# Optimization experiments

Hardware: AMD Instinct MI355X
Metric: run time of the kernel (lower is better)

Reference implementation:

```python
import jax, jax.numpy as jnp
import numpy as np

NHID = 1024
NTOKEN = 10000
T, B = 128, 32
INITRANGE = 0.04
# DARTS recurrent genotype: (activation, predecessor-state index)
GENO = (("sigmoid", 0), ("relu", 1), ("relu", 1), ("identity", 1),
        ("tanh", 2), ("sigmoid", 5), ("tanh", 3), ("relu", 5))
CONCAT = tuple(range(1, 9))
ACT = {"sigmoid": jax.nn.sigmoid, "relu": jax.nn.relu,
       "tanh": jnp.tanh, "identity": lambda x: x}


def setup_inputs() -> dict:
    key = jax.random.key(0)
    ks = jax.random.split(key, 4)
    u = lambda k, shape: jax.random.uniform(k, shape, jnp.float32, -INITRANGE, INITRANGE)
    return {
        "tokens": jax.random.randint(ks[0], (T, B), 0, NTOKEN),
        "h0": jnp.zeros((B, NHID), jnp.float32),
        "enc_W": u(ks[1], (NTOKEN, NHID)),            # tied encoder/decoder weight
        "W0": u(ks[2], (2 * NHID, 2 * NHID)),          # (ninp+nhid, 2*nhid)
        "Ws": u(ks[3], (len(GENO), NHID, 2 * NHID)),   # one matrix per genotype edge
        "dec_b": jnp.zeros((NTOKEN,), jnp.float32),
    }


def _cell(x, h_prev, W0, Ws):
    # init state: c0,h0 from cat(x, h_prev) @ W0
    xh = jnp.concatenate([x, h_prev], axis=-1)           # (B, 2*nhid)
    c0, h0 = jnp.split(xh @ W0, 2, axis=-1)
    s = h_prev + jax.nn.sigmoid(c0) * (jnp.tanh(h0) - h_prev)
    states = [s]
    for i, (name, pred) in enumerate(GENO):
        sp = states[pred]
        c, h = jnp.split(sp @ Ws[i], 2, axis=-1)
        states.append(sp + jax.nn.sigmoid(c) * (ACT[name](h) - sp))
    # output = mean over concat states
    return sum(states[i] for i in CONCAT) / float(len(CONCAT))


def reference(tokens, h0, enc_W, W0, Ws, dec_b):
    emb = enc_W[tokens]                                  # (T, B, ninp)

    def step(h, x):
        h_new = _cell(x, h, W0, Ws)
        return h_new, h_new

    h_last, hiddens = jax.lax.scan(step, h0, emb)        # hiddens: (T, B, nhid)
    logits = hiddens @ enc_W.T + dec_b                   # tied decoder (T, B, ntoken)
    log_prob = jax.nn.log_softmax(logits, axis=-1)
    return log_prob, h_last[None]                        # ((T,B,V), (1,B,nhid))
```

## Files before the change

### kernel.cpp

```cpp
#include <hip/hip_runtime.h>
#include <cmath>

#define NHID 1024
#define NTOK 10000
#define TT 128
#define BB 32
#define BN (BB*NHID)
#define WMAT (2048*1024)
#define FSTRIDE 16

typedef __attribute__((ext_vector_type(8))) short s8v;
typedef __attribute__((ext_vector_type(4))) float f4v;

#define MFMA(a,b,c) __builtin_amdgcn_mfma_f32_16x16x32_bf16(a,b,c,0,0,0)

__device__ __forceinline__ float sigf(float x){ return 1.f/(1.f+__expf(-x)); }
__device__ __forceinline__ float actf(int a, float h){
  switch(a){ case 0: return sigf(h); case 1: return fmaxf(h,0.f);
             case 2: return tanhf(h); default: return h; }
}
__device__ __forceinline__ unsigned short f2bf(float x){
  union { float f; unsigned u; } v; v.f = x;
  unsigned r = v.u + 0x7fffu + ((v.u >> 16) & 1u);
  return (unsigned short)(r >> 16);
}

__device__ __forceinline__ void ld_f2(const float* p, float& x0, float& x1){
  unsigned long long u = __hip_atomic_load((const unsigned long long*)p,
                         __ATOMIC_RELAXED, __HIP_MEMORY_SCOPE_AGENT);
  union { unsigned long long u; float f[2]; } v; v.u = u;
  x0 = v.f[0]; x1 = v.f[1];
}

__device__ __forceinline__ void coh_ld16(const unsigned short* pa, const unsigned short* pb,
                                         s8v A[8], s8v B[8]){
  asm volatile(
    "global_load_dwordx4 %0, %16, off sc0 sc1\n\t"
    "global_load_dwordx4 %1, %16, off offset:64 sc0 sc1\n\t"
    "global_load_dwordx4 %2, %16, off offset:128 sc0 sc1\n\t"
    "global_load_dwordx4 %3, %16, off offset:192 sc0 sc1\n\t"
    "global_load_dwordx4 %4, %16, off offset:256 sc0 sc1\n\t"
    "global_load_dwordx4 %5, %16, off offset:320 sc0 sc1\n\t"
    "global_load_dwordx4 %6, %16, off offset:384 sc0 sc1\n\t"
    "global_load_dwordx4 %7, %16, off offset:448 sc0 sc1\n\t"
    "global_load_dwordx4 %8, %17, off sc0 sc1\n\t"
    "global_load_dwordx4 %9, %17, off offset:64 sc0 sc1\n\t"
    "global_load_dwordx4 %10, %17, off offset:128 sc0 sc1\n\t"
    "global_load_dwordx4 %11, %17, off offset:192 sc0 sc1\n\t"
    "global_load_dwordx4 %12, %17, off offset:256 sc0 sc1\n\t"
    "global_load_dwordx4 %13, %17, off offset:320 sc0 sc1\n\t"
    "global_load_dwordx4 %14, %17, off offset:384 sc0 sc1\n\t"
    "global_load_dwordx4 %15, %17, off offset:448 sc0 sc1\n\t"
    "s_waitcnt vmcnt(0)"
    : "=&v"(A[0]),"=&v"(A[1]),"=&v"(A[2]),"=&v"(A[3]),
      "=&v"(A[4]),"=&v"(A[5]),"=&v"(A[6]),"=&v"(A[7]),
      "=&v"(B[0]),"=&v"(B[1]),"=&v"(B[2]),"=&v"(B[3]),
      "=&v"(B[4]),"=&v"(B[5]),"=&v"(B[6]),"=&v"(B[7])
    : "v"(pa), "v"(pb)
    : "memory");
}

__device__ __forceinline__ void st_wt32(void* p, unsigned x){
  asm volatile("global_store_dword %0, %1, off sc0 sc1" :: "v"(p), "v"(x) : "memory");
}
__device__ __forceinline__ void st_wt64(void* p, unsigned long long x){
  asm volatile("global_store_dwordx2 %0, %1, off sc0 sc1" :: "v"(p), "v"(x) : "memory");
}
__device__ __forceinline__ unsigned long long packf2(float a, float b){
  union { float f[2]; unsigned long long u; } v; v.f[0]=a; v.f[1]=b; return v.u;
}


__global__ __launch_bounds__(256) void k_transpose_cvt(
    const float* __restrict__ W0, const float* __restrict__ Ws,
    unsigned short* __restrict__ dstAll)
{
  int z = blockIdx.z;
  const float* src = (z==0) ? W0 : (z==1) ? (W0 + (size_t)1024*2048)
                                          : (Ws + (size_t)(z-2)*1024*2048);
  unsigned short* dst = dstAll + (size_t)z*WMAT;
  __shared__ float tile[32][33];
  int n0 = blockIdx.x*32;
  int k0 = blockIdx.y*32;
  int tx = threadIdx.x & 31, ty = threadIdx.x >> 5;
  #pragma unroll
  for (int i=0;i<4;i++){
    int k = k0 + ty + i*8;
    tile[ty + i*8][tx] = src[(size_t)k*2048 + n0 + tx];
  }
  __syncthreads();
  #pragma unroll
  for (int i=0;i<4;i++){
    int n = n0 + ty + i*8;
    dst[(size_t)n*1024 + k0 + tx] = f2bf(tile[tx][ty + i*8]);
  }
}

__global__ void k_cvt(const float* __restrict__ src, unsigned short* __restrict__ dst, int n){
  int i = blockIdx.x*blockDim.x + threadIdx.x;
  int stride = gridDim.x*blockDim.x;
  for (; i < n; i += stride) dst[i] = f2bf(src[i]);
}

__global__ void k_zero(unsigned* __restrict__ p, int n){
  int i = blockIdx.x*blockDim.x + threadIdx.x;
  if (i < n) p[i] = 0u;
}


__device__ __forceinline__ void poll1(const unsigned* F, int idx, unsigned tgt){
  const unsigned* f = F + (size_t)idx*FSTRIDE;
  while (__hip_atomic_load(f, __ATOMIC_RELAXED, __HIP_MEMORY_SCOPE_AGENT) < tgt)
    __builtin_amdgcn_s_sleep(2);
}
__device__ __forceinline__ void signal(unsigned* F, int s, int tile, unsigned val){
  asm volatile("s_waitcnt vmcnt(0)" ::: "memory");
  __syncthreads();
  if (threadIdx.x == 0)
    st_wt32((void*)(F + (size_t)((s<<6)+tile)*FSTRIDE), val);
}

struct B8 { s8v c[8]; s8v h[8]; };

__device__ __forceinline__ void load_b8(const unsigned short* __restrict__ Wt,
                                        int z, int j0, int r, int kb, int q, B8& B){
  const unsigned short* wz = Wt + (size_t)z*WMAT;
  const s8v* bc = (const s8v*)(wz + (size_t)(j0+r)*1024 + kb);
  const s8v* bh = (const s8v*)(wz + (size_t)(1024+j0+r)*1024 + kb);
  #pragma unroll
  for (int i=0;i<8;i++){ B.c[i]=bc[q+4*i]; B.h[i]=bh[q+4*i]; }
}

__device__ __forceinline__ void do_edge_reg(
    const B8& B, float* __restrict__ st_f,
    unsigned short* __restrict__ st_bf, float* __restrict__ red,
    unsigned* __restrict__ F, int pred, int outs, int act,
    int j0, int tile, unsigned tgt, int wave, int q, int r, int tid)
{
  int lane = tid & 63;
  if (lane < 17){
    int idx = (pred<<6) + ((lane<16) ? (wave*16 + lane) : tile);
    poll1(F, idx, tgt);
  }
  int row = tid>>3, col = (tid&7)*2;
  size_t off = (size_t)row*NHID + j0 + col;
  float sp0, sp1;
  ld_f2(st_f + (size_t)pred*BN + off, sp0, sp1);
  const unsigned short* spb = st_bf + (size_t)pred*BN;
  int kb = wave*256;
  s8v a0[8], a1[8];
  coh_ld16(spb + (size_t)r*NHID + kb + q*8,
           spb + (size_t)(16+r)*NHID + kb + q*8, a0, a1);
  f4v zz = {0.f,0.f,0.f,0.f};
  f4v aC0=zz,aC1=zz,aH0=zz,aH1=zz;
  #pragma unroll
  for (int i=0;i<8;i++){
    aC0=MFMA(a0[i],B.c[i],aC0); aC1=MFMA(a1[i],B.c[i],aC1);
    aH0=MFMA(a0[i],B.h[i],aH0); aH1=MFMA(a1[i],B.h[i],aH1);
  }
  #pragma unroll
  for (int i=0;i<4;i++){
    red[((wave*4+0)*32 + q*4+i)*16 + r]    = aC0[i];
    red[((wave*4+0)*32 + 16+q*4+i)*16 + r] = aC1[i];
    red[((wave*4+1)*32 + q*4+i)*16 + r]    = aH0[i];
    red[((wave*4+1)*32 + 16+q*4+i)*16 + r] = aH1[i];
  }
  __syncthreads();
  float cs0=0,cs1=0,hs0=0,hs1=0;
  #pragma unroll
  for (int w2=0; w2<4; w2++){
    cs0 += red[((w2*4+0)*32+row)*16+col];
    cs1 += red[((w2*4+0)*32+row)*16+col+1];
    hs0 += red[((w2*4+1)*32+row)*16+col];
    hs1 += red[((w2*4+1)*32+row)*16+col+1];
  }
  float v0 = sp0 + sigf(cs0)*(actf(act,hs0) - sp0);
  float v1 = sp1 + sigf(cs1)*(actf(act,hs1) - sp1);
  st_wt64(&st_f[(size_t)outs*BN+off], packf2(v0, v1));
  unsigned pk = (unsigned)f2bf(v0) | ((unsigned)f2bf(v1)<<16);
  st_wt32((unsigned*)(st_bf + (size_t)outs*BN + off), pk);
  signal(F, outs, tile, tgt);
}

__global__ __launch_bounds__(256, 1) void k_recur(
    const int* __restrict__ tok, const float* __restrict__ h0f,
    const unsigned short* __restrict__ encb,
    const unsigned short* __restrict__ Wt,
    const unsigned short* __restrict__ h0b,
    float* __restrict__ st_f, unsigned short* __restrict__ st_bf,
    float* __restrict__ h_f, unsigned short* __restrict__ h_bf,
    unsigned short* __restrict__ hid_bf, unsigned* __restrict__ F)
{
  __shared__ float red[4*4*32*16];
  int wg = blockIdx.x, grp = wg >> 6, tile = wg & 63;
  int tid = threadIdx.x, wave = tid>>6, lane = tid&63, q = lane>>4, r = lane&15;
  int j0 = tile * 16;

  if (grp == 0) {
    B8 BX; load_b8(Wt, 0, j0, r, wave*256, q, BX);
    B8 BH; load_b8(Wt, 1, j0, r, wave*256, q, BH);
    B8 B3; load_b8(Wt, 5, j0, r, wave*256, q, B3);

    for (int t = 0; t < TT; ++t) {
      unsigned tgt = t+1;
      s8v xa0[8], xa1[8];
      {
        int kb = wave * 256;
        const s8v* e0p = (const s8v*)(encb + (size_t)tok[t*BB + r]*NHID + kb);
        const s8v* e1p = (const s8v*)(encb + (size_t)tok[t*BB + 16 + r]*NHID + kb);
        #pragma unroll
        for (int i=0;i<8;i++){ xa0[i]=e0p[q+4*i]; xa1[i]=e1p[q+4*i]; }
      }
      if (t && lane < 17){
        int idx = (8<<6) + ((lane<16) ? (wave*16 + lane) : tile);
        poll1(F, idx, t);
      }
      int row = tid>>3, col = (tid&7)*2;
      size_t off = (size_t)row*NHID + j0 + col;
      const float* hfb = t ? h_f : h0f;
      float hp0, hp1; ld_f2(hfb + off, hp0, hp1);
      const unsigned short* hb = t ? h_bf : h0b;
      int kb = wave*256;
      s8v ha0[8], ha1[8];
      coh_ld16(hb + (size_t)r*NHID + kb + q*8,
               hb + (size_t)(16+r)*NHID + kb + q*8, ha0, ha1);
      f4v zz = {0.f,0.f,0.f,0.f};
      f4v aC0=zz,aC1=zz,aH0=zz,aH1=zz;
      #pragma unroll
      for (int i=0;i<8;i++){
        aC0=MFMA(xa0[i],BX.c[i],aC0); aC1=MFMA(xa1[i],BX.c[i],aC1);
        aH0=MFMA(xa0[i],BX.h[i],aH0); aH1=MFMA(xa1[i],BX.h[i],aH1);
      }
      #pragma unroll
      for (int i=0;i<8;i++){
        aC0=MFMA(ha0[i],BH.c[i],aC0); aC1=MFMA(ha1[i],BH.c[i],aC1);
        aH0=MFMA(ha0[i],BH.h[i],aH0); aH1=MFMA(ha1[i],BH.h[i],aH1);
      }
      #pragma unroll
      for (int i=0;i<4;i++){
        red[((wave*4+0)*32 + q*4+i)*16 + r]    = aC0[i];
        red[((wave*4+0)*32 + 16+q*4+i)*16 + r] = aC1[i];
        red[((wave*4+1)*32 + q*4+i)*16 + r]    = aH0[i];
        red[((wave*4+1)*32 + 16+q*4+i)*16 + r] = aH1[i];
      }
      __syncthreads();
      float cs0=0,cs1=0,hs0=0,hs1=0;
      #pragma unroll
      for (int w2=0; w2<4; w2++){
        cs0 += red[((w2*4+0)*32+row)*16+col];
        cs1 += red[((w2*4+0)*32+row)*16+col+1];
        hs0 += red[((w2*4+1)*32+row)*16+col];
        hs1 += red[((w2*4+1)*32+row)*16+col+1];
      }
      float v0 = hp0 + sigf(cs0)*(tanhf(hs0)-hp0);
      float v1 = hp1 + sigf(cs1)*(tanhf(hs1)-hp1);
      st_wt64(&st_f[off], packf2(v0, v1));
      unsigned pk = (unsigned)f2bf(v0) | ((unsigned)f2bf(v1)<<16);
      st_wt32((unsigned*)(st_bf + off), pk);
      signal(F, 0, tile, tgt);
      do_edge_reg(B3, st_f, st_bf, red, F, 1, 4, 3, j0, tile, tgt, wave, q, r, tid);
    }
  } else if (grp == 1) {
    B8 B0; load_b8(Wt, 2, j0, r, wave*256, q, B0);
    B8 B4; load_b8(Wt, 6, j0, r, wave*256, q, B4);
    for (int t = 0; t < TT; ++t) {
      unsigned tgt = t+1;
      do_edge_reg(B0, st_f, st_bf, red, F, 0, 1, 0, j0, tile, tgt, wave, q, r, tid);
      do_edge_reg(B4, st_f, st_bf, red, F, 2, 5, 2, j0, tile, tgt, wave, q, r, tid);
    }
  } else if (grp == 2) {
    B8 B1; load_b8(Wt, 3, j0, r, wave*256, q, B1);
    B8 B6; load_b8(Wt, 8, j0, r, wave*256, q, B6);
    for (int t = 0; t < TT; ++t) {
      unsigned tgt = t+1;
      do_edge_reg(B1, st_f, st_bf, red, F, 1, 2, 1, j0, tile, tgt, wave, q, r, tid);
      do_edge_reg(B6, st_f, st_bf, red, F, 3, 7, 2, j0, tile, tgt, wave, q, r, tid);
    }
  } else {
    B8 B2; load_b8(Wt, 4, j0, r, wave*256, q, B2);
    B8 B5; load_b8(Wt, 7, j0, r, wave*256, q, B5);
    B8 B7; load_b8(Wt, 9, j0, r, wave*256, q, B7);
    for (int t = 0; t < TT; ++t) {
      unsigned tgt = t+1;
      do_edge_reg(B2, st_f, st_bf, red, F, 1, 3, 1, j0, tile, tgt, wave, q, r, tid);
      if (lane < 19){
        int idx = (lane<16) ? ((5<<6) + wave*16 + lane)
                : (lane==16) ? ((4<<6)+tile)
                : (lane==17) ? ((5<<6)+tile) : ((7<<6)+tile);
        poll1(F, idx, tgt);
      }
      {
        int row = tid>>3, col = (tid&7)*2;
        size_t off = (size_t)row*NHID + j0 + col;
        float s1a,s1b,s2a,s2b,s3a,s3b,s4a,s4b,s5a,s5b,s7a,s7b;
        ld_f2(st_f + (size_t)1*BN + off, s1a, s1b);
        ld_f2(st_f + (size_t)2*BN + off, s2a, s2b);
        ld_f2(st_f + (size_t)3*BN + off, s3a, s3b);
        ld_f2(st_f + (size_t)4*BN + off, s4a, s4b);
        ld_f2(st_f + (size_t)5*BN + off, s5a, s5b);
        ld_f2(st_f + (size_t)7*BN + off, s7a, s7b);
        const unsigned short* spb = st_bf + (size_t)5*BN;
        int kb = wave*256;
        s8v a0[8], a1[8];
        coh_ld16(spb + (size_t)r*NHID + kb + q*8,
                 spb + (size_t)(16+r)*NHID + kb + q*8, a0, a1);
        f4v zz = {0.f,0.f,0.f,0.f};
        f4v c50=zz,c51=zz,h50=zz,h51=zz,c70=zz,c71=zz,h70=zz,h71=zz;
        #pragma unroll
        for (int i=0;i<8;i++){
          c50=MFMA(a0[i],B5.c[i],c50); c51=MFMA(a1[i],B5.c[i],c51);
          h50=MFMA(a0[i],B5.h[i],h50); h51=MFMA(a1[i],B5.h[i],h51);
          c70=MFMA(a0[i],B7.c[i],c70); c71=MFMA(a1[i],B7.c[i],c71);
          h70=MFMA(a0[i],B7.h[i],h70); h71=MFMA(a1[i],B7.h[i],h71);
        }
        #pragma unroll
        for (int i=0;i<4;i++){
          red[((wave*4+0)*32 + q*4+i)*16 + r]    = c50[i];
          red[((wave*4+0)*32 + 16+q*4+i)*16 + r] = c51[i];
          red[((wave*4+1)*32 + q*4+i)*16 + r]    = h50[i];
          red[((wave*4+1)*32 + 16+q*4+i)*16 + r] = h51[i];
          red[((wave*4+2)*32 + q*4+i)*16 + r]    = c70[i];
          red[((wave*4+2)*32 + 16+q*4+i)*16 + r] = c71[i];
          red[((wave*4+3)*32 + q*4+i)*16 + r]    = h70[i];
          red[((wave*4+3)*32 + 16+q*4+i)*16 + r] = h71[i];
        }
        __syncthreads();
        float a5c[2]={0,0}, a5h[2]={0,0}, a7c[2]={0,0}, a7h[2]={0,0};
        #pragma unroll
        for (int w2=0; w2<4; w2++){
          #pragma unroll
          for (int u=0; u<2; u++){
            a5c[u] += red[((w2*4+0)*32+row)*16+col+u];
            a5h[u] += red[((w2*4+1)*32+row)*16+col+u];
            a7c[u] += red[((w2*4+2)*32+row)*16+col+u];
            a7h[u] += red[((w2*4+3)*32+row)*16+col+u];
          }
        }
        float s5v[2] = {s5a, s5b};
        float o1[2] = {s1a, s1b}, o2[2] = {s2a, s2b}, o3[2] = {s3a, s3b};
        float o4[2] = {s4a, s4b}, o7[2] = {s7a, s7b};
        float hv[2];
        #pragma unroll
        for (int u=0; u<2; u++){
          float s5j = s5v[u];
          float s6 = s5j + sigf(a5c[u])*(sigf(a5h[u]) - s5j);
          float s8 = s5j + sigf(a7c[u])*(fmaxf(a7h[u],0.f) - s5j);
          float sum = o1[u] + o2[u] + o3[u] + o4[u]
                    + s5j + s6 + o7[u] + s8;
          hv[u] = 0.125f * sum;
        }
        st_wt64(&h_f[off], packf2(hv[0], hv[1]));
        unsigned pk = (unsigned)f2bf(hv[0]) | ((unsigned)f2bf(hv[1])<<16);
        st_wt32((unsigned*)(h_bf + off), pk);
        *(unsigned*)(hid_bf + (size_t)t*BN + off) = pk;
        signal(F, 8, tile, tgt);
      }
    }
  }
}


__global__ __launch_bounds__(256) void k_decoder(
    const unsigned short* __restrict__ Hb, const unsigned short* __restrict__ Wb,
    float* __restrict__ out)
{
  int L = blockIdx.x;
  int xcd = L & 7, i = L >> 3;
  int band = i / 320;
  int r2 = i % 320;
  int bnIdx = r2 >> 4, bmi = r2 & 15;
  int bn_t = xcd + 8*bnIdx;
  if (bn_t >= 157) return;
  int bm_t = band*16 + bmi;
  int wave = threadIdx.x >> 6, lane = threadIdx.x & 63;
  int q = lane >> 4, r = lane & 15;
  int bm = bm_t*64 + (wave>>1)*32;
  int bn = bn_t*64 + (wave&1)*32;
  f4v z = {0.f,0.f,0.f,0.f};
  f4v acc00=z, acc01=z, acc10=z, acc11=z;
  const s8v* a0p = (const s8v*)(Hb + (size_t)(bm + r)*NHID);
  const s8v* a1p = (const s8v*)(Hb + (size_t)(bm + 16 + r)*NHID);
  int n0 = bn + r, n1 = bn + 16 + r;
  const s8v* b0p = (const s8v*)(Wb + (size_t)(n0 < NTOK ? n0 : 0)*NHID);
  const s8v* b1p = (const s8v*)(Wb + (size_t)(n1 < NTOK ? n1 : 0)*NHID);
  #pragma unroll 4
  for (int v = q; v < 128; v += 4) {
    s8v a0 = a0p[v], a1 = a1p[v], b0 = b0p[v], b1 = b1p[v];
    acc00 = MFMA(a0, b0, acc00); acc10 = MFMA(a1, b0, acc10);
    acc01 = MFMA(a0, b1, acc01); acc11 = MFMA(a1, b1, acc11);
  }
  #pragma unroll
  for (int ni=0; ni<2; ni++){
    int col = bn + ni*16 + r;
    if (col >= NTOK) continue;
    #pragma unroll
    for (int mi=0; mi<2; mi++){
      f4v a = (mi==0) ? (ni==0 ? acc00 : acc01) : (ni==0 ? acc10 : acc11);
      #pragma unroll
      for (int t4=0; t4<4; t4++){
        int row = bm + mi*16 + q*4 + t4;
        out[(size_t)row*NTOK + col] = a[t4];
      }
    }
  }
}

__global__ __launch_bounds__(256) void k_logsoftmax(
    float* __restrict__ logits, const float* __restrict__ bias)
{
  size_t row = blockIdx.x;
  float* p = logits + row * NTOK;
  float v[40];
  float mx = -1e30f;
  #pragma unroll
  for (int i=0;i<40;i++){
    int c = threadIdx.x + (i<<8);
    float x = (c < NTOK) ? (p[c] + bias[c]) : -1e30f;
    v[i] = x; mx = fmaxf(mx, x);
  }
  #pragma unroll
  for (int off=32; off>0; off>>=1) mx = fmaxf(mx, __shfl_down(mx, off));
  __shared__ float red[4], red2[4];
  int wv = threadIdx.x>>6, ln = threadIdx.x&63;
  if (ln==0) red[wv] = mx;
  __syncthreads();
  mx = fmaxf(fmaxf(red[0],red[1]), fmaxf(red[2],red[3]));
  float s = 0.f;
  #pragma unroll
  for (int i=0;i<40;i++) s += __expf(v[i] - mx);
  #pragma unroll
  for (int off=32; off>0; off>>=1) s += __shfl_down(s, off);
  if (ln==0) red2[wv] = s;
  __syncthreads();
  s = red2[0]+red2[1]+red2[2]+red2[3];
  float lse = mx + __logf(s);
  #pragma unroll
  for (int i=0;i<40;i++){
    int c = threadIdx.x + (i<<8);
    if (c < NTOK) p[c] = v[i] - lse;
  }
}

__global__ void k_copy(const float* __restrict__ src, float* __restrict__ dst, int n){
  int i = blockIdx.x*blockDim.x + threadIdx.x;
  if (i < n) dst[i] = src[i];
}


extern "C" void kernel_launch(void* const* d_in, const int* in_sizes, int n_in,
                              void* d_out, int out_size, void* d_ws, size_t ws_size,
                              hipStream_t stream) {
  const int*   tok  = (const int*)d_in[0];
  const float* h0   = (const float*)d_in[1];
  const float* encw = (const float*)d_in[2];
  const float* W0   = (const float*)d_in[3];
  const float* Ws   = (const float*)d_in[4];
  const float* decb = (const float*)d_in[5];
  float* out = (float*)d_out;

  char* w = (char*)d_ws;
  unsigned short* Wt      = (unsigned short*)w; w += (size_t)10*WMAT*2;
  unsigned short* encw_bf = (unsigned short*)w; w += (size_t)NTOK*NHID*2;
  unsigned short* h0_bf   = (unsigned short*)w; w += (size_t)BN*2;
  unsigned short* hid_bf  = (unsigned short*)w; w += (size_t)TT*BN*2;
  float*          st_f    = (float*)w;          w += (size_t)9*BN*4;
  unsigned short* st_bf   = (unsigned short*)w; w += (size_t)9*BN*2;
  float*          h_f     = (float*)w;          w += (size_t)BN*4;
  unsigned short* h_bf    = (unsigned short*)w; w += (size_t)BN*2;
  unsigned*       flags   = (unsigned*)w;       w += (size_t)576*FSTRIDE*4;

  k_zero<<<36, 256, 0, stream>>>(flags, 576*FSTRIDE);
  k_transpose_cvt<<<dim3(64,32,10), 256, 0, stream>>>(W0, Ws, Wt);
  k_cvt<<<4096, 256, 0, stream>>>(encw, encw_bf, NTOK*NHID);
  k_cvt<<<128, 256, 0, stream>>>(h0, h0_bf, BN);

  k_recur<<<256, 256, 0, stream>>>(tok, h0, encw_bf, Wt, h0_bf,
                                   st_f, st_bf, h_f, h_bf, hid_bf, flags);

  k_decoder<<<10240, 256, 0, stream>>>(hid_bf, encw_bf, out);
  k_logsoftmax<<<TT*BB, 256, 0, stream>>>(out, decb);
  k_copy<<<128, 256, 0, stream>>>(h_f, out + (size_t)TT*BB*NTOK, BN);
}
```

Before: 3.553 ms.

## Fuse the three edges sharing state 1 into one group and widen decoder tiles

The three genotype edges that all read state 1 (edges 1, 2, 3) now run together in one workgroup group. It loads the state-1 activations once, issues MFMAs against three register-resident weight matrices, reduces six channels through a larger LDS buffer, and signals three flags at once. Edge 6 moves to group 0 to rebalance the work, which shortens the per-timestep dependency chain and saves two flag round trips. The decoder GEMM switches to a 64x128 block tile with a plain 2D grid, replacing the XCD-swizzled 64x64 mapping, and the poll sleep is shortened. Costs include more VGPR pressure from holding three B8 weight sets and the loss of the XCD-aware L2 locality in the decoder.

```diff
diff --git a/kernel.cpp b/kernel.cpp
--- a/kernel.cpp
+++ b/kernel.cpp
@@ -8,6 +8,7 @@
 #define BN (BB*NHID)
 #define WMAT (2048*1024)
 #define FSTRIDE 16
+#define CHST 6
 
 typedef __attribute__((ext_vector_type(8))) short s8v;
 typedef __attribute__((ext_vector_type(4))) float f4v;
@@ -111,7 +112,7 @@
 __device__ __forceinline__ void poll1(const unsigned* F, int idx, unsigned tgt){
   const unsigned* f = F + (size_t)idx*FSTRIDE;
   while (__hip_atomic_load(f, __ATOMIC_RELAXED, __HIP_MEMORY_SCOPE_AGENT) < tgt)
-    __builtin_amdgcn_s_sleep(2);
+    __builtin_amdgcn_s_sleep(1);
 }
 __device__ __forceinline__ void signal(unsigned* F, int s, int tile, unsigned val){
   asm volatile("s_waitcnt vmcnt(0)" ::: "memory");
@@ -160,19 +161,19 @@
   }
   #pragma unroll
   for (int i=0;i<4;i++){
-    red[((wave*4+0)*32 + q*4+i)*16 + r]    = aC0[i];
-    red[((wave*4+0)*32 + 16+q*4+i)*16 + r] = aC1[i];
-    red[((wave*4+1)*32 + q*4+i)*16 + r]    = aH0[i];
-    red[((wave*4+1)*32 + 16+q*4+i)*16 + r] = aH1[i];
+    red[((wave*CHST+0)*32 + q*4+i)*16 + r]    = aC0[i];
+    red[((wave*CHST+0)*32 + 16+q*4+i)*16 + r] = aC1[i];
+    red[((wave*CHST+1)*32 + q*4+i)*16 + r]    = aH0[i];
+    red[((wave*CHST+1)*32 + 16+q*4+i)*16 + r] = aH1[i];
   }
   __syncthreads();
   float cs0=0,cs1=0,hs0=0,hs1=0;
   #pragma unroll
   for (int w2=0; w2<4; w2++){
-    cs0 += red[((w2*4+0)*32+row)*16+col];
-    cs1 += red[((w2*4+0)*32+row)*16+col+1];
-    hs0 += red[((w2*4+1)*32+row)*16+col];
-    hs1 += red[((w2*4+1)*32+row)*16+col+1];
+    cs0 += red[((w2*CHST+0)*32+row)*16+col];
+    cs1 += red[((w2*CHST+0)*32+row)*16+col+1];
+    hs0 += red[((w2*CHST+1)*32+row)*16+col];
+    hs1 += red[((w2*CHST+1)*32+row)*16+col+1];
   }
   float v0 = sp0 + sigf(cs0)*(actf(act,hs0) - sp0);
   float v1 = sp1 + sigf(cs1)*(actf(act,hs1) - sp1);
@@ -191,7 +192,7 @@
     float* __restrict__ h_f, unsigned short* __restrict__ h_bf,
     unsigned short* __restrict__ hid_bf, unsigned* __restrict__ F)
 {
-  __shared__ float red[4*4*32*16];
+  __shared__ float red[4*CHST*32*16];
   int wg = blockIdx.x, grp = wg >> 6, tile = wg & 63;
   int tid = threadIdx.x, wave = tid>>6, lane = tid&63, q = lane>>4, r = lane&15;
   int j0 = tile * 16;
@@ -199,7 +200,7 @@
   if (grp == 0) {
     B8 BX; load_b8(Wt, 0, j0, r, wave*256, q, BX);
     B8 BH; load_b8(Wt, 1, j0, r, wave*256, q, BH);
-    B8 B3; load_b8(Wt, 5, j0, r, wave*256, q, B3);
+    B8 B6; load_b8(Wt, 8, j0, r, wave*256, q, B6);
 
     for (int t = 0; t < TT; ++t) {
       unsigned tgt = t+1;
@@ -238,19 +239,19 @@
       }
       #pragma unroll
       for (int i=0;i<4;i++){
-        red[((wave*4+0)*32 + q*4+i)*16 + r]    = aC0[i];
-        red[((wave*4+0)*32 + 16+q*4+i)*16 + r] = aC1[i];
-        red[((wave*4+1)*32 + q*4+i)*16 + r]    = aH0[i];
-        red[((wave*4+1)*32 + 16+q*4+i)*16 + r] = aH1[i];
+        red[((wave*CHST+0)*32 + q*4+i)*16 + r]    = aC0[i];
+        red[((wave*CHST+0)*32 + 16+q*4+i)*16 + r] = aC1[i];
+        red[((wave*CHST+1)*32 + q*4+i)*16 + r]    = aH0[i];
+        red[((wave*CHST+1)*32 + 16+q*4+i)*16 + r] = aH1[i];
       }
       __syncthreads();
       float cs0=0,cs1=0,hs0=0,hs1=0;
       #pragma unroll
       for (int w2=0; w2<4; w2++){
-        cs0 += red[((w2*4+0)*32+row)*16+col];
-        cs1 += red[((w2*4+0)*32+row)*16+col+1];
-        hs0 += red[((w2*4+1)*32+row)*16+col];
-        hs1 += red[((w2*4+1)*32+row)*16+col+1];
+        cs0 += red[((w2*CHST+0)*32+row)*16+col];
+        cs1 += red[((w2*CHST+0)*32+row)*16+col+1];
+        hs0 += red[((w2*CHST+1)*32+row)*16+col];
+        hs1 += red[((w2*CHST+1)*32+row)*16+col+1];
       }
       float v0 = hp0 + sigf(cs0)*(tanhf(hs0)-hp0);
       float v1 = hp1 + sigf(cs1)*(tanhf(hs1)-hp1);
@@ -258,7 +259,7 @@
       unsigned pk = (unsigned)f2bf(v0) | ((unsigned)f2bf(v1)<<16);
       st_wt32((unsigned*)(st_bf + off), pk);
       signal(F, 0, tile, tgt);
-      do_edge_reg(B3, st_f, st_bf, red, F, 1, 4, 3, j0, tile, tgt, wave, q, r, tid);
+      do_edge_reg(B6, st_f, st_bf, red, F, 3, 7, 2, j0, tile, tgt, wave, q, r, tid);
     }
   } else if (grp == 1) {
     B8 B0; load_b8(Wt, 2, j0, r, wave*256, q, B0);
@@ -270,19 +271,94 @@
     }
   } else if (grp == 2) {
     B8 B1; load_b8(Wt, 3, j0, r, wave*256, q, B1);
-    B8 B6; load_b8(Wt, 8, j0, r, wave*256, q, B6);
+    B8 B2; load_b8(Wt, 4, j0, r, wave*256, q, B2);
+    B8 B3; load_b8(Wt, 5, j0, r, wave*256, q, B3);
     for (int t = 0; t < TT; ++t) {
       unsigned tgt = t+1;
-      do_edge_reg(B1, st_f, st_bf, red, F, 1, 2, 1, j0, tile, tgt, wave, q, r, tid);
-      do_edge_reg(B6, st_f, st_bf, red, F, 3, 7, 2, j0, tile, tgt, wave, q, r, tid);
+      if (lane < 17){
+        int idx = (1<<6) + ((lane<16) ? (wave*16 + lane) : tile);
+        poll1(F, idx, tgt);
+      }
+      int row = tid>>3, col = (tid&7)*2;
+      size_t off = (size_t)row*NHID + j0 + col;
+      float sp0, sp1;
+      ld_f2(st_f + (size_t)1*BN + off, sp0, sp1);
+      const unsigned short* spb = st_bf + (size_t)1*BN;
+      int kb = wave*256;
+      s8v a0[8], a1[8];
+      coh_ld16(spb + (size_t)r*NHID + kb + q*8,
+               spb + (size_t)(16+r)*NHID + kb + q*8, a0, a1);
+      f4v zz = {0.f,0.f,0.f,0.f};
+      f4v c10=zz,c11=zz,h10=zz,h11=zz;
+      f4v c20=zz,c21=zz,h20=zz,h21=zz;
+      f4v c30=zz,c31=zz,h30=zz,h31=zz;
+      #pragma unroll
+      for (int i=0;i<8;i++){
+        s8v x0=a0[i], x1=a1[i];
+        c10=MFMA(x0,B1.c[i],c10); c11=MFMA(x1,B1.c[i],c11);
+        h10=MFMA(x0,B1.h[i],h10); h11=MFMA(x1,B1.h[i],h11);
+        c20=MFMA(x0,B2.c[i],c20); c21=MFMA(x1,B2.c[i],c21);
+        h20=MFMA(x0,B2.h[i],h20); h21=MFMA(x1,B2.h[i],h21);
+        c30=MFMA(x0,B3.c[i],c30); c31=MFMA(x1,B3.c[i],c31);
+        h30=MFMA(x0,B3.h[i],h30); h31=MFMA(x1,B3.h[i],h31);
+      }
+      #pragma unroll
+      for (int i=0;i<4;i++){
+        red[((wave*CHST+0)*32 + q*4+i)*16 + r]    = c10[i];
+        red[((wave*CHST+0)*32 + 16+q*4+i)*16 + r] = c11[i];
+        red[((wave*CHST+1)*32 + q*4+i)*16 + r]    = h10[i];
+        red[((wave*CHST+1)*32 + 16+q*4+i)*16 + r] = h11[i];
+        red[((wave*CHST+2)*32 + q*4+i)*16 + r]    = c20[i];
+        red[((wave*CHST+2)*32 + 16+q*4+i)*16 + r] = c21[i];
+        red[((wave*CHST+3)*32 + q*4+i)*16 + r]    = h20[i];
+        red[((wave*CHST+3)*32 + 16+q*4+i)*16 + r] = h21[i];
+        red[((wave*CHST+4)*32 + q*4+i)*16 + r]    = c30[i];
+        red[((wave*CHST+4)*32 + 16+q*4+i)*16 + r] = c31[i];
+        red[((wave*CHST+5)*32 + q*4+i)*16 + r]    = h30[i];
+        red[((wave*CHST+5)*32 + 16+q*4+i)*16 + r] = h31[i];
+      }
+      __syncthreads();
+      float s[6][2];
+      #pragma unroll
+      for (int ch=0; ch<6; ch++){ s[ch][0]=0.f; s[ch][1]=0.f; }
+      #pragma unroll
+      for (int w2=0; w2<4; w2++){
+        #pragma unroll
+        for (int ch=0; ch<6; ch++){
+          s[ch][0] += red[((w2*CHST+ch)*32+row)*16+col];
+          s[ch][1] += red[((w2*CHST+ch)*32+row)*16+col+1];
+        }
+      }
+      float spv[2] = {sp0, sp1};
+      float v2[2], v3[2], v4[2];
+      #pragma unroll
+      for (int u=0; u<2; u++){
+        float sp = spv[u];
+        v2[u] = sp + sigf(s[0][u])*(fmaxf(s[1][u],0.f) - sp);
+        v3[u] = sp + sigf(s[2][u])*(fmaxf(s[3][u],0.f) - sp);
+        v4[u] = sp + sigf(s[4][u])*(s[5][u] - sp);
+      }
+      st_wt64(&st_f[(size_t)2*BN+off], packf2(v2[0], v2[1]));
+      st_wt64(&st_f[(size_t)3*BN+off], packf2(v3[0], v3[1]));
+      st_wt64(&st_f[(size_t)4*BN+off], packf2(v4[0], v4[1]));
+      unsigned pk2 = (unsigned)f2bf(v2[0]) | ((unsigned)f2bf(v2[1])<<16);
+      unsigned pk3 = (unsigned)f2bf(v3[0]) | ((unsigned)f2bf(v3[1])<<16);
+      unsigned pk4 = (unsigned)f2bf(v4[0]) | ((unsigned)f2bf(v4[1])<<16);
+      st_wt32((unsigned*)(st_bf + (size_t)2*BN + off), pk2);
+      st_wt32((unsigned*)(st_bf + (size_t)3*BN + off), pk3);
+      st_wt32((unsigned*)(st_bf + (size_t)4*BN + off), pk4);
+      asm volatile("s_waitcnt vmcnt(0)" ::: "memory");
+      __syncthreads();
+      if (threadIdx.x < 3){
+        int ss = 2 + threadIdx.x;
+        st_wt32((void*)(F + (size_t)((ss<<6)+tile)*FSTRIDE), tgt);
+      }
     }
   } else {
-    B8 B2; load_b8(Wt, 4, j0, r, wave*256, q, B2);
     B8 B5; load_b8(Wt, 7, j0, r, wave*256, q, B5);
     B8 B7; load_b8(Wt, 9, j0, r, wave*256, q, B7);
     for (int t = 0; t < TT; ++t) {
       unsigned tgt = t+1;
-      do_edge_reg(B2, st_f, st_bf, red, F, 1, 3, 1, j0, tile, tgt, wave, q, r, tid);
       if (lane < 19){
         int idx = (lane<16) ? ((5<<6) + wave*16 + lane)
                 : (lane==16) ? ((4<<6)+tile)
@@ -315,14 +391,14 @@
         }
         #pragma unroll
         for (int i=0;i<4;i++){
-          red[((wave*4+0)*32 + q*4+i)*16 + r]    = c50[i];
-          red[((wave*4+0)*32 + 16+q*4+i)*16 + r] = c51[i];
-          red[((wave*4+1)*32 + q*4+i)*16 + r]    = h50[i];
-          red[((wave*4+1)*32 + 16+q*4+i)*16 + r] = h51[i];
-          red[((wave*4+2)*32 + q*4+i)*16 + r]    = c70[i];
-          red[((wave*4+2)*32 + 16+q*4+i)*16 + r] = c71[i];
-          red[((wave*4+3)*32 + q*4+i)*16 + r]    = h70[i];
-          red[((wave*4+3)*32 + 16+q*4+i)*16 + r] = h71[i];
+          red[((wave*CHST+0)*32 + q*4+i)*16 + r]    = c50[i];
+          red[((wave*CHST+0)*32 + 16+q*4+i)*16 + r] = c51[i];
+          red[((wave*CHST+1)*32 + q*4+i)*16 + r]    = h50[i];
+          red[((wave*CHST+1)*32 + 16+q*4+i)*16 + r] = h51[i];
+          red[((wave*CHST+2)*32 + q*4+i)*16 + r]    = c70[i];
+          red[((wave*CHST+2)*32 + 16+q*4+i)*16 + r] = c71[i];
+          red[((wave*CHST+3)*32 + q*4+i)*16 + r]    = h70[i];
+          red[((wave*CHST+3)*32 + 16+q*4+i)*16 + r] = h71[i];
         }
         __syncthreads();
         float a5c[2]={0,0}, a5h[2]={0,0}, a7c[2]={0,0}, a7h[2]={0,0};
@@ -330,10 +406,10 @@
         for (int w2=0; w2<4; w2++){
           #pragma unroll
           for (int u=0; u<2; u++){
-            a5c[u] += red[((w2*4+0)*32+row)*16+col+u];
-            a5h[u] += red[((w2*4+1)*32+row)*16+col+u];
-            a7c[u] += red[((w2*4+2)*32+row)*16+col+u];
-            a7h[u] += red[((w2*4+3)*32+row)*16+col+u];
+            a5c[u] += red[((w2*CHST+0)*32+row)*16+col+u];
+            a5h[u] += red[((w2*CHST+1)*32+row)*16+col+u];
+            a7c[u] += red[((w2*CHST+2)*32+row)*16+col+u];
+            a7h[u] += red[((w2*CHST+3)*32+row)*16+col+u];
           }
         }
         float s5v[2] = {s5a, s5b};
@@ -364,43 +440,44 @@
     const unsigned short* __restrict__ Hb, const unsigned short* __restrict__ Wb,
     float* __restrict__ out)
 {
-  int L = blockIdx.x;
-  int xcd = L & 7, i = L >> 3;
-  int band = i / 320;
-  int r2 = i % 320;
-  int bnIdx = r2 >> 4, bmi = r2 & 15;
-  int bn_t = xcd + 8*bnIdx;
-  if (bn_t >= 157) return;
-  int bm_t = band*16 + bmi;
-  int wave = threadIdx.x >> 6, lane = threadIdx.x & 63;
+  int wv = threadIdx.x >> 6, lane = threadIdx.x & 63;
   int q = lane >> 4, r = lane & 15;
-  int bm = bm_t*64 + (wave>>1)*32;
-  int bn = bn_t*64 + (wave&1)*32;
-  f4v z = {0.f,0.f,0.f,0.f};
-  f4v acc00=z, acc01=z, acc10=z, acc11=z;
+  int bm = blockIdx.y*64 + (wv&1)*32;
+  int bn = blockIdx.x*128 + (wv>>1)*64;
   const s8v* a0p = (const s8v*)(Hb + (size_t)(bm + r)*NHID);
   const s8v* a1p = (const s8v*)(Hb + (size_t)(bm + 16 + r)*NHID);
-  int n0 = bn + r, n1 = bn + 16 + r;
-  const s8v* b0p = (const s8v*)(Wb + (size_t)(n0 < NTOK ? n0 : 0)*NHID);
-  const s8v* b1p = (const s8v*)(Wb + (size_t)(n1 < NTOK ? n1 : 0)*NHID);
+  const s8v* bp0; const s8v* bp1; const s8v* bp2; const s8v* bp3;
+  {
+    int c0 = bn + r,      c1 = bn + 16 + r;
+    int c2 = bn + 32 + r, c3 = bn + 48 + r;
+    bp0 = (const s8v*)(Wb + (size_t)(c0 < NTOK ? c0 : 0)*NHID);
+    bp1 = (const s8v*)(Wb + (size_t)(c1 < NTOK ? c1 : 0)*NHID);
+    bp2 = (const s8v*)(Wb + (size_t)(c2 < NTOK ? c2 : 0)*NHID);
+    bp3 = (const s8v*)(Wb + (size_t)(c3 < NTOK ? c3 : 0)*NHID);
+  }
+  f4v z = {0.f,0.f,0.f,0.f};
+  f4v acc00=z,acc01=z,acc02=z,acc03=z;
+  f4v acc10=z,acc11=z,acc12=z,acc13=z;
   #pragma unroll 4
   for (int v = q; v < 128; v += 4) {
-    s8v a0 = a0p[v], a1 = a1p[v], b0 = b0p[v], b1 = b1p[v];
+    s8v a0 = a0p[v], a1 = a1p[v];
+    s8v b0 = bp0[v], b1 = bp1[v], b2 = bp2[v], b3 = bp3[v];
     acc00 = MFMA(a0, b0, acc00); acc10 = MFMA(a1, b0, acc10);
     acc01 = MFMA(a0, b1, acc01); acc11 = MFMA(a1, b1, acc11);
-  }
-  #pragma unroll
-  for (int ni=0; ni<2; ni++){
-    int col = bn + ni*16 + r;
+    acc02 = MFMA(a0, b2, acc02); acc12 = MFMA(a1, b2, acc12);
+    acc03 = MFMA(a0, b3, acc03); acc13 = MFMA(a1, b3, acc13);
+  }
+  #pragma unroll
+  for (int n=0; n<4; n++){
+    int col = bn + n*16 + r;
     if (col >= NTOK) continue;
+    f4v am0 = (n==0)?acc00:(n==1)?acc01:(n==2)?acc02:acc03;
+    f4v am1 = (n==0)?acc10:(n==1)?acc11:(n==2)?acc12:acc13;
     #pragma unroll
-    for (int mi=0; mi<2; mi++){
-      f4v a = (mi==0) ? (ni==0 ? acc00 : acc01) : (ni==0 ? acc10 : acc11);
-      #pragma unroll
-      for (int t4=0; t4<4; t4++){
-        int row = bm + mi*16 + q*4 + t4;
-        out[(size_t)row*NTOK + col] = a[t4];
-      }
+    for (int i=0; i<4; i++){
+      int row0 = bm + q*4 + i;
+      out[(size_t)row0*NTOK + col]      = am0[i];
+      out[(size_t)(row0+16)*NTOK + col] = am1[i];
     }
   }
 }
@@ -477,7 +554,7 @@
   k_recur<<<256, 256, 0, stream>>>(tok, h0, encw_bf, Wt, h0_bf,
                                    st_f, st_bf, h_f, h_bf, hid_bf, flags);
 
-  k_decoder<<<10240, 256, 0, stream>>>(hid_bf, encw_bf, out);
+  k_decoder<<<dim3(79,64), 256, 0, stream>>>(hid_bf, encw_bf, out);
   k_logsoftmax<<<TT*BB, 256, 0, stream>>>(out, decb);
   k_copy<<<128, 256, 0, stream>>>(h_f, out + (size_t)TT*BB*NTOK, BN);
 }
```

Result: no change. 3.556 ms (+0.1%).
